# Kernel tuning notes

Hardware: AMD Instinct MI355X
Metric: run time of the kernel (lower is better)

Reference implementation:

```python
import jax, jax.numpy as jnp
import numpy as np

N, E, D_IN, D_H = 50000, 800000, 128, 128


def setup_inputs() -> dict:
    key = jax.random.key(0)
    ks = jax.random.split(key, 8)
    x = jax.random.normal(ks[0], (N, D_IN), dtype=jnp.float32)
    edge_index = jax.random.randint(ks[1], (2, E), 0, N, dtype=jnp.int64)
    edge_attr = jax.random.normal(ks[2], (E, D_H), dtype=jnp.float32)
    s_in = 1.0 / np.sqrt(D_IN)
    W_mean = jax.random.uniform(ks[3], (D_H, D_IN), jnp.float32, -s_in, s_in)
    b_mean = jax.random.uniform(ks[4], (D_H,), jnp.float32, -s_in, s_in)
    W_std = jax.random.uniform(ks[5], (D_H, D_IN), jnp.float32, -s_in, s_in)
    b_std = jax.random.uniform(ks[6], (D_H,), jnp.float32, -s_in, s_in)
    return {"x": x, "edge_index": edge_index, "edge_attr": edge_attr,
            "W_mean": W_mean, "b_mean": b_mean, "W_std": W_std, "b_std": b_std}


def _gcn(x, edge_index, edge_attr, W, b):
    # linear projection: [N, D_H]
    h = x @ W.T + b
    row, col = edge_index[0], edge_index[1]
    n = x.shape[0]
    # degree of target nodes (col), symmetric-ish normalization
    deg = jax.ops.segment_sum(jnp.ones(row.shape[0], dtype=h.dtype), col, num_segments=n)
    deg_inv_sqrt = jnp.where(deg > 0, jax.lax.rsqrt(jnp.maximum(deg, 1.0)) * jnp.where(deg > 0, 1.0, 0.0), 0.0)
    norm = deg_inv_sqrt[row] * deg_inv_sqrt[col]  # [E]
    msg = norm[:, None] * (h[row] + edge_attr)     # [E, D_H]
    out = jax.ops.segment_sum(msg, col, num_segments=n) + h  # aggregate at target + residual
    return out


def reference(x, edge_index, edge_attr, W_mean, b_mean, W_std, b_std):
    mean = _gcn(x, edge_index, edge_attr, W_mean, b_mean)
    std = _gcn(x, edge_index, edge_attr, W_std, b_std)
    return (mean, std)
```

## Files before the change

### kernel.cpp

```cpp
#include <hip/hip_runtime.h>
#include <math.h>

#define N_NODES 50000
#define N_EDGES 800000
#define D 128

static __device__ __forceinline__ unsigned short f2bf(float f) {
    unsigned u = __float_as_uint(f);
    u += 0x7FFFu + ((u >> 16) & 1u);
    return (unsigned short)(u >> 16);
}

__global__ __launch_bounds__(256) void zero_kernel(int* __restrict__ p, int n) {
    int i = blockIdx.x * blockDim.x + threadIdx.x;
    if (i < n) p[i] = 0;
}

__global__ __launch_bounds__(256) void hist_kernel(const int* __restrict__ ei,
                                                   int* __restrict__ count) {
    int e = blockIdx.x * blockDim.x + threadIdx.x;
    if (e < N_EDGES) {
        atomicAdd(&count[ei[N_EDGES + e]], 1);
    }
}

__global__ __launch_bounds__(1024) void scan1_kernel(const int* __restrict__ count,
                                                     int* __restrict__ offset,
                                                     float* __restrict__ dis,
                                                     int* __restrict__ bsum) {
    __shared__ int wsum[16];
    const int tid = threadIdx.x;
    const int lane = tid & 63;
    const int wid = tid >> 6;
    const int i = blockIdx.x * 1024 + tid;

    int c = (i < N_NODES) ? count[i] : 0;
    int inc = c;
#pragma unroll
    for (int d = 1; d < 64; d <<= 1) {
        int v = __shfl_up(inc, d, 64);
        if (lane >= d) inc += v;
    }
    if (lane == 63) wsum[wid] = inc;
    __syncthreads();
    if (wid == 0) {
        int s = (lane < 16) ? wsum[lane] : 0;
#pragma unroll
        for (int d = 1; d < 16; d <<= 1) {
            int v = __shfl_up(s, d, 64);
            if (lane >= d) s += v;
        }
        if (lane < 16) wsum[lane] = s;
    }
    __syncthreads();
    int wpre = (wid > 0) ? wsum[wid - 1] : 0;
    if (i < N_NODES) {
        offset[i] = wpre + inc - c;
        dis[i] = (c > 0) ? rsqrtf((float)c) : 0.0f;
    }
    if (tid == 0) bsum[blockIdx.x] = wsum[15];
}

__global__ __launch_bounds__(1024) void fixup_kernel(const int* __restrict__ bsum,
                                                     int* __restrict__ offset,
                                                     int* __restrict__ cur) {
    __shared__ int pre_s;
    const int tid = threadIdx.x;
    const int blk = blockIdx.x;
    if ((tid >> 6) == 0) {
        int lane = tid & 63;
        int s = 0;
        for (int j = lane; j < blk; j += 64) s += bsum[j];
#pragma unroll
        for (int d = 32; d > 0; d >>= 1) s += __shfl_xor(s, d, 64);
        if (lane == 0) pre_s = s;
    }
    __syncthreads();
    int i = blk * 1024 + tid;
    if (i < N_NODES) {
        int o = offset[i] + pre_s;
        offset[i] = o;
        cur[i] = o;
    }
}

__global__ __launch_bounds__(256) void scatter_kernel(const int* __restrict__ ei,
                                                      const float* __restrict__ dis,
                                                      int* __restrict__ cur,
                                                      int4* __restrict__ meta) {
    int e = blockIdx.x * blockDim.x + threadIdx.x;
    if (e < N_EDGES) {
        int row = ei[e];
        int col = ei[N_EDGES + e];
        int p = atomicAdd(&cur[col], 1);
        meta[p] = make_int4(e, row, __float_as_int(dis[row]), 0);
    }
}

#define TILE_R 32
__global__ __launch_bounds__(256) void gemm_kernel(
    const float* __restrict__ x,
    const float* __restrict__ Wm, const float* __restrict__ bm,
    const float* __restrict__ Ws, const float* __restrict__ bs,
    float* __restrict__ h, ushort2* __restrict__ hpk)
{
    __shared__ float xs[TILE_R][D];
    const int r0 = blockIdx.x * TILE_R;
    const int tid = threadIdx.x;

    for (int i = tid; i < TILE_R * D / 4; i += 256) {
        int rr = i / (D / 4);
        int cc = (i % (D / 4)) * 4;
        int r = r0 + rr;
        float4 v = make_float4(0.f, 0.f, 0.f, 0.f);
        if (r < N_NODES) v = *(const float4*)(x + (size_t)r * D + cc);
        *(float4*)(&xs[rr][cc]) = v;
    }
    __syncthreads();

    const int m = tid >> 7;
    const int p = (tid >> 1) & 63;
    const int rh = tid & 1;
    const int c0 = p * 2;
    const float* __restrict__ W = m ? Ws : Wm;
    const float* __restrict__ b = m ? bs : bm;
    const float b0 = b[c0], b1 = b[c0 + 1];

    float acc0[16], acc1[16];
#pragma unroll
    for (int rr = 0; rr < 16; ++rr) { acc0[rr] = b0; acc1[rr] = b1; }

    const float* __restrict__ Wr0 = W + (size_t)c0 * D;
    const float* __restrict__ Wr1 = W + (size_t)(c0 + 1) * D;

    for (int kc = 0; kc < D; kc += 32) {
        float w0[32], w1[32];
#pragma unroll
        for (int j = 0; j < 32; j += 4) {
            float4 a = *(const float4*)(Wr0 + kc + j);
            float4 bb = *(const float4*)(Wr1 + kc + j);
            w0[j] = a.x; w0[j+1] = a.y; w0[j+2] = a.z; w0[j+3] = a.w;
            w1[j] = bb.x; w1[j+1] = bb.y; w1[j+2] = bb.z; w1[j+3] = bb.w;
        }
#pragma unroll
        for (int rr = 0; rr < 16; ++rr) {
            const float* xr = &xs[rh * 16 + rr][kc];
#pragma unroll
            for (int j = 0; j < 32; j += 4) {
                float4 xv = *(const float4*)(xr + j);
                acc0[rr] = fmaf(xv.x, w0[j],     acc0[rr]);
                acc0[rr] = fmaf(xv.y, w0[j + 1], acc0[rr]);
                acc0[rr] = fmaf(xv.z, w0[j + 2], acc0[rr]);
                acc0[rr] = fmaf(xv.w, w0[j + 3], acc0[rr]);
                acc1[rr] = fmaf(xv.x, w1[j],     acc1[rr]);
                acc1[rr] = fmaf(xv.y, w1[j + 1], acc1[rr]);
                acc1[rr] = fmaf(xv.z, w1[j + 2], acc1[rr]);
                acc1[rr] = fmaf(xv.w, w1[j + 3], acc1[rr]);
            }
        }
    }

    const size_t hb = (size_t)m * N_NODES * D;
#pragma unroll
    for (int rr = 0; rr < 16; ++rr) {
        int r = r0 + rh * 16 + rr;
        if (r < N_NODES) {
            float2 v; v.x = acc0[rr]; v.y = acc1[rr];
            *(float2*)(h + hb + (size_t)r * D + c0) = v;
            ushort2 u; u.x = f2bf(acc0[rr]); u.y = f2bf(acc1[rr]);
            hpk[(size_t)r * 128 + p * 2 + m] = u;
        }
    }
}

__global__ __launch_bounds__(256) void agg_kernel(
    const float* __restrict__ ea, const uint2* __restrict__ hpk,
    const int4* __restrict__ meta,
    const int* __restrict__ offset, const int* __restrict__ cur,
    const float* __restrict__ dis,
    const float* __restrict__ hm, const float* __restrict__ hs,
    float* __restrict__ om, float* __restrict__ os)
{
    const int tid = threadIdx.x;
    const int lane = tid & 63;
    const int wid = tid >> 6;
    const int n = blockIdx.x * 4 + wid;

    const int start = offset[n];
    const int end = cur[n];
    const float dc = dis[n];
    const int k = lane * 2;

    float amx = 0.f, amy = 0.f, asx = 0.f, asy = 0.f;

    for (int jb = start; jb < end; jb += 64) {
        int4 mt = make_int4(0, 0, 0, 0);
        if (jb + lane < end) mt = meta[jb + lane];
        const int mm = min(64, end - jb);

        int e0   = __builtin_amdgcn_readlane(mt.x, 0);
        int row0 = __builtin_amdgcn_readlane(mt.y, 0);
        float dr_c = __int_as_float(__builtin_amdgcn_readlane(mt.z, 0));
        float2 ea_c = *(const float2*)(ea + (size_t)e0 * D + k);
        uint2  hp_c = hpk[(size_t)row0 * 64 + lane];

        for (int j = 0; j < mm; ++j) {
            const int jn = (j + 1 < mm) ? (j + 1) : j;
            int e1   = __builtin_amdgcn_readlane(mt.x, jn);
            int row1 = __builtin_amdgcn_readlane(mt.y, jn);
            float dr_n = __int_as_float(__builtin_amdgcn_readlane(mt.z, jn));
            float2 ea_n = *(const float2*)(ea + (size_t)e1 * D + k);
            uint2  hp_n = hpk[(size_t)row1 * 64 + lane];

            float h0 = __uint_as_float(hp_c.x << 16);
            float h1 = __uint_as_float(hp_c.x & 0xFFFF0000u);
            float g0 = __uint_as_float(hp_c.y << 16);
            float g1 = __uint_as_float(hp_c.y & 0xFFFF0000u);

            amx = fmaf(dr_c, h0 + ea_c.x, amx);
            amy = fmaf(dr_c, h1 + ea_c.y, amy);
            asx = fmaf(dr_c, g0 + ea_c.x, asx);
            asy = fmaf(dr_c, g1 + ea_c.y, asy);

            ea_c = ea_n; hp_c = hp_n; dr_c = dr_n;
        }
    }

    const size_t ob = (size_t)n * D + k;
    float2 hmn = *(const float2*)(hm + ob);
    float2 hsn = *(const float2*)(hs + ob);
    float2 o0, o1;
    o0.x = hmn.x + dc * amx;  o0.y = hmn.y + dc * amy;
    o1.x = hsn.x + dc * asx;  o1.y = hsn.y + dc * asy;
    *(float2*)(om + ob) = o0;
    *(float2*)(os + ob) = o1;
}

extern "C" void kernel_launch(void* const* d_in, const int* in_sizes, int n_in,
                              void* d_out, int out_size, void* d_ws, size_t ws_size,
                              hipStream_t stream) {
    const float* x   = (const float*)d_in[0];
    const int*   ei  = (const int*)d_in[1];
    const float* ea  = (const float*)d_in[2];
    const float* Wm  = (const float*)d_in[3];
    const float* bm  = (const float*)d_in[4];
    const float* Ws  = (const float*)d_in[5];
    const float* bs  = (const float*)d_in[6];
    float* out = (float*)d_out;

    char* w = (char*)d_ws;
    int*   count  = (int*)w;     w += (size_t)N_NODES * 4;
    int*   offset = (int*)w;     w += (size_t)N_NODES * 4;
    int*   cur    = (int*)w;     w += (size_t)N_NODES * 4;
    float* dis    = (float*)w;   w += (size_t)N_NODES * 4;
    int*   bsum   = (int*)w;     w += 4096;
    int4*  meta   = (int4*)w;    w += (size_t)N_EDGES * 16;
    float* h      = (float*)w;   w += (size_t)2 * N_NODES * D * 4;
    ushort2* hpk  = (ushort2*)w;
    float* hm = h;
    float* hs = h + (size_t)N_NODES * D;

    float* om = out;
    float* os = out + (size_t)N_NODES * D;

    const int SCAN_BLKS = (N_NODES + 1023) / 1024;

    zero_kernel<<<(N_NODES + 255) / 256, 256, 0, stream>>>(count, N_NODES);

    hist_kernel<<<(N_EDGES + 255) / 256, 256, 0, stream>>>(ei, count);

    scan1_kernel<<<SCAN_BLKS, 1024, 0, stream>>>(count, offset, dis, bsum);
    fixup_kernel<<<SCAN_BLKS, 1024, 0, stream>>>(bsum, offset, cur);

    scatter_kernel<<<(N_EDGES + 255) / 256, 256, 0, stream>>>(ei, dis, cur, meta);

    gemm_kernel<<<(N_NODES + TILE_R - 1) / TILE_R, 256, 0, stream>>>(
        x, Wm, bm, Ws, bs, h, (ushort2*)hpk);

    agg_kernel<<<N_NODES / 4, 256, 0, stream>>>(ea, (const uint2*)hpk, meta,
                                                offset, cur, dis, hm, hs, om, os);
}
```

Before: 301.1 us.

## Fuse scatter into GEMM launch, deepen agg prefetch, add nontemporal loads

Merges the edge-scatter kernel and the projection GEMM into one launch whose extra blocks do the scatter, so the two independent stages can overlap and one launch is saved. The zero kernel becomes hipMemsetAsync. The aggregation loop now prefetches two edges ahead instead of one, uses nontemporal loads and stores for edge attributes, metadata and outputs, and loads the residual before the loop. These changes aim to hide gather latency and avoid polluting the cache, at the cost of more registers and a mix of very different block types in one launch.

```diff
diff --git a/kernel.cpp b/kernel.cpp
--- a/kernel.cpp
+++ b/kernel.cpp
@@ -4,16 +4,15 @@
 #define N_NODES 50000
 #define N_EDGES 800000
 #define D 128
+
+typedef float        vf2 __attribute__((ext_vector_type(2)));
+typedef unsigned int vu2 __attribute__((ext_vector_type(2)));
+typedef int          vi4 __attribute__((ext_vector_type(4)));
 
 static __device__ __forceinline__ unsigned short f2bf(float f) {
     unsigned u = __float_as_uint(f);
     u += 0x7FFFu + ((u >> 16) & 1u);
     return (unsigned short)(u >> 16);
-}
-
-__global__ __launch_bounds__(256) void zero_kernel(int* __restrict__ p, int n) {
-    int i = blockIdx.x * blockDim.x + threadIdx.x;
-    if (i < n) p[i] = 0;
 }
 
 __global__ __launch_bounds__(256) void hist_kernel(const int* __restrict__ ei,
@@ -84,29 +83,32 @@
     }
 }
 
-__global__ __launch_bounds__(256) void scatter_kernel(const int* __restrict__ ei,
-                                                      const float* __restrict__ dis,
-                                                      int* __restrict__ cur,
-                                                      int4* __restrict__ meta) {
-    int e = blockIdx.x * blockDim.x + threadIdx.x;
-    if (e < N_EDGES) {
-        int row = ei[e];
-        int col = ei[N_EDGES + e];
-        int p = atomicAdd(&cur[col], 1);
-        meta[p] = make_int4(e, row, __float_as_int(dis[row]), 0);
-    }
-}
-
 #define TILE_R 32
-__global__ __launch_bounds__(256) void gemm_kernel(
+#define GEMM_BLKS ((N_NODES + TILE_R - 1) / TILE_R)
+#define SCAT_BLKS ((N_EDGES + 255) / 256)
+__global__ __launch_bounds__(256) void fused_kernel(
     const float* __restrict__ x,
     const float* __restrict__ Wm, const float* __restrict__ bm,
     const float* __restrict__ Ws, const float* __restrict__ bs,
-    float* __restrict__ h, ushort2* __restrict__ hpk)
+    float* __restrict__ h, ushort2* __restrict__ hpk,
+    const int* __restrict__ ei, const float* __restrict__ dis,
+    int* __restrict__ cur, int4* __restrict__ meta)
 {
     __shared__ float xs[TILE_R][D];
+    const int tid = threadIdx.x;
+
+    if (blockIdx.x >= GEMM_BLKS) {
+        int e = (blockIdx.x - GEMM_BLKS) * 256 + tid;
+        if (e < N_EDGES) {
+            int row = ei[e];
+            int col = ei[N_EDGES + e];
+            int p = atomicAdd(&cur[col], 1);
+            meta[p] = make_int4(e, row, __float_as_int(dis[row]), 0);
+        }
+        return;
+    }
+
     const int r0 = blockIdx.x * TILE_R;
-    const int tid = threadIdx.x;
 
     for (int i = tid; i < TILE_R * D / 4; i += 256) {
         int rr = i / (D / 4);
@@ -174,7 +176,7 @@
 }
 
 __global__ __launch_bounds__(256) void agg_kernel(
-    const float* __restrict__ ea, const uint2* __restrict__ hpk,
+    const float* __restrict__ ea, const vu2* __restrict__ hpk,
     const int4* __restrict__ meta,
     const int* __restrict__ offset, const int* __restrict__ cur,
     const float* __restrict__ dis,
@@ -191,49 +193,59 @@
     const float dc = dis[n];
     const int k = lane * 2;
 
+    const size_t ob = (size_t)n * D + k;
+    vf2 hmn = __builtin_nontemporal_load((const vf2*)(hm + ob));
+    vf2 hsn = __builtin_nontemporal_load((const vf2*)(hs + ob));
+
     float amx = 0.f, amy = 0.f, asx = 0.f, asy = 0.f;
 
     for (int jb = start; jb < end; jb += 64) {
-        int4 mt = make_int4(0, 0, 0, 0);
-        if (jb + lane < end) mt = meta[jb + lane];
+        vi4 mt = (vi4)(0);
+        if (jb + lane < end)
+            mt = __builtin_nontemporal_load((const vi4*)(meta + jb + lane));
         const int mm = min(64, end - jb);
 
-        int e0   = __builtin_amdgcn_readlane(mt.x, 0);
-        int row0 = __builtin_amdgcn_readlane(mt.y, 0);
-        float dr_c = __int_as_float(__builtin_amdgcn_readlane(mt.z, 0));
-        float2 ea_c = *(const float2*)(ea + (size_t)e0 * D + k);
-        uint2  hp_c = hpk[(size_t)row0 * 64 + lane];
+        int   eA = __builtin_amdgcn_readlane(mt[0], 0);
+        int   rA = __builtin_amdgcn_readlane(mt[1], 0);
+        float dA = __int_as_float(__builtin_amdgcn_readlane(mt[2], 0));
+        vf2 eaA = __builtin_nontemporal_load((const vf2*)(ea + (size_t)eA * D + k));
+        vu2 hpA = hpk[(size_t)rA * 64 + lane];
+
+        const int j1 = (mm > 1) ? 1 : 0;
+        int   eB = __builtin_amdgcn_readlane(mt[0], j1);
+        int   rB = __builtin_amdgcn_readlane(mt[1], j1);
+        float dB = __int_as_float(__builtin_amdgcn_readlane(mt[2], j1));
+        vf2 eaB = __builtin_nontemporal_load((const vf2*)(ea + (size_t)eB * D + k));
+        vu2 hpB = hpk[(size_t)rB * 64 + lane];
 
         for (int j = 0; j < mm; ++j) {
-            const int jn = (j + 1 < mm) ? (j + 1) : j;
-            int e1   = __builtin_amdgcn_readlane(mt.x, jn);
-            int row1 = __builtin_amdgcn_readlane(mt.y, jn);
-            float dr_n = __int_as_float(__builtin_amdgcn_readlane(mt.z, jn));
-            float2 ea_n = *(const float2*)(ea + (size_t)e1 * D + k);
-            uint2  hp_n = hpk[(size_t)row1 * 64 + lane];
-
-            float h0 = __uint_as_float(hp_c.x << 16);
-            float h1 = __uint_as_float(hp_c.x & 0xFFFF0000u);
-            float g0 = __uint_as_float(hp_c.y << 16);
-            float g1 = __uint_as_float(hp_c.y & 0xFFFF0000u);
-
-            amx = fmaf(dr_c, h0 + ea_c.x, amx);
-            amy = fmaf(dr_c, h1 + ea_c.y, amy);
-            asx = fmaf(dr_c, g0 + ea_c.x, asx);
-            asy = fmaf(dr_c, g1 + ea_c.y, asy);
-
-            ea_c = ea_n; hp_c = hp_n; dr_c = dr_n;
-        }
-    }
-
-    const size_t ob = (size_t)n * D + k;
-    float2 hmn = *(const float2*)(hm + ob);
-    float2 hsn = *(const float2*)(hs + ob);
-    float2 o0, o1;
-    o0.x = hmn.x + dc * amx;  o0.y = hmn.y + dc * amy;
-    o1.x = hsn.x + dc * asx;  o1.y = hsn.y + dc * asy;
-    *(float2*)(om + ob) = o0;
-    *(float2*)(os + ob) = o1;
+            const int jn = (j + 2 < mm) ? (j + 2) : (mm - 1);
+            int   eN = __builtin_amdgcn_readlane(mt[0], jn);
+            int   rN = __builtin_amdgcn_readlane(mt[1], jn);
+            float dN = __int_as_float(__builtin_amdgcn_readlane(mt[2], jn));
+            vf2 eaN = __builtin_nontemporal_load((const vf2*)(ea + (size_t)eN * D + k));
+            vu2 hpN = hpk[(size_t)rN * 64 + lane];
+
+            float h0 = __uint_as_float(hpA[0] << 16);
+            float h1 = __uint_as_float(hpA[0] & 0xFFFF0000u);
+            float g0 = __uint_as_float(hpA[1] << 16);
+            float g1 = __uint_as_float(hpA[1] & 0xFFFF0000u);
+
+            amx = fmaf(dA, h0 + eaA[0], amx);
+            amy = fmaf(dA, h1 + eaA[1], amy);
+            asx = fmaf(dA, g0 + eaA[0], asx);
+            asy = fmaf(dA, g1 + eaA[1], asy);
+
+            eaA = eaB; hpA = hpB; dA = dB;
+            eaB = eaN; hpB = hpN; dB = dN;
+        }
+    }
+
+    vf2 o0, o1;
+    o0[0] = hmn[0] + dc * amx;  o0[1] = hmn[1] + dc * amy;
+    o1[0] = hsn[0] + dc * asx;  o1[1] = hsn[1] + dc * asy;
+    __builtin_nontemporal_store(o0, (vf2*)(om + ob));
+    __builtin_nontemporal_store(o1, (vf2*)(os + ob));
 }
 
 extern "C" void kernel_launch(void* const* d_in, const int* in_sizes, int n_in,
@@ -265,18 +277,16 @@
 
     const int SCAN_BLKS = (N_NODES + 1023) / 1024;
 
-    zero_kernel<<<(N_NODES + 255) / 256, 256, 0, stream>>>(count, N_NODES);
-
-    hist_kernel<<<(N_EDGES + 255) / 256, 256, 0, stream>>>(ei, count);
+    hipMemsetAsync(count, 0, N_NODES * sizeof(int), stream);
+
+    hist_kernel<<<SCAT_BLKS, 256, 0, stream>>>(ei, count);
 
     scan1_kernel<<<SCAN_BLKS, 1024, 0, stream>>>(count, offset, dis, bsum);
     fixup_kernel<<<SCAN_BLKS, 1024, 0, stream>>>(bsum, offset, cur);
 
-    scatter_kernel<<<(N_EDGES + 255) / 256, 256, 0, stream>>>(ei, dis, cur, meta);
-
-    gemm_kernel<<<(N_NODES + TILE_R - 1) / TILE_R, 256, 0, stream>>>(
-        x, Wm, bm, Ws, bs, h, (ushort2*)hpk);
-
-    agg_kernel<<<N_NODES / 4, 256, 0, stream>>>(ea, (const uint2*)hpk, meta,
+    fused_kernel<<<GEMM_BLKS + SCAT_BLKS, 256, 0, stream>>>(
+        x, Wm, bm, Ws, bs, h, hpk, ei, dis, cur, meta);
+
+    agg_kernel<<<N_NODES / 4, 256, 0, stream>>>(ea, (const vu2*)hpk, meta,
                                                 offset, cur, dis, hm, hs, om, os);
 }
```

Result: faster. 267.8 us (-11.1%).
